# Kernel optimization log

Hardware: AMD Instinct MI355X
Metric: run time of the kernel (lower is better)

## Reference

```python
import jax, jax.numpy as jnp
import numpy as np

B, S, H, HD, DIM = 4, 4096, 32, 128, 4096
INTER = 11008
HC = 32          # heavy_channel_num
POS = 3000       # decode position
HEAVY = 256      # heavy_const (top-k keys kept)
BASE = 40000.0   # rope_base
EPS = 1e-5


def setup_inputs() -> dict:
    key = jax.random.key(0)
    ks = jax.random.split(key, 12)
    x = jax.random.normal(ks[0], (B, 1, DIM), jnp.float32)
    wqkv = jax.random.normal(ks[1], (3 * DIM, DIM), jnp.float32) * 0.02
    wo = jax.random.normal(ks[2], (DIM, DIM), jnp.float32) * 0.02
    w1 = jax.random.normal(ks[3], (INTER, DIM), jnp.float32) * 0.02
    w2 = jax.random.normal(ks[4], (DIM, INTER), jnp.float32) * 0.02
    w3 = jax.random.normal(ks[5], (INTER, DIM), jnp.float32) * 0.02
    attn_norm_w = jnp.ones((DIM,), jnp.float32)
    ffn_norm_w = jnp.ones((DIM,), jnp.float32)
    k_cache = jax.random.normal(ks[6], (B, S, H, HD), jnp.float32)
    v_cache = jax.random.normal(ks[7], (B, S, H, HD), jnp.float32)
    sorted_channel = jax.random.randint(ks[8], (H, HC), 0, HD).astype(jnp.int32)
    # k_label cache is consistent with k_cache gathered at the heavy channels
    k_label_cache = jnp.take_along_axis(k_cache, sorted_channel[None, None, :, :], axis=3)
    # rope freqs for the single decode position: [1, HD//2, 2] (cos, sin)
    inv = 1.0 / (BASE ** (np.arange(0, HD, 2, dtype=np.float32) / HD))
    ang = POS * inv
    freqs_cis = jnp.asarray(np.stack([np.cos(ang), np.sin(ang)], -1)[None], jnp.float32)
    # causal mask over cache positions (0 for valid, -1e9 beyond current pos)
    mask1 = jnp.where(jnp.arange(S) <= POS, 0.0, -1e9).astype(jnp.float32).reshape(1, 1, 1, S)
    return dict(x=x, wqkv=wqkv, wo=wo, w1=w1, w2=w2, w3=w3,
                attn_norm_w=attn_norm_w, ffn_norm_w=ffn_norm_w,
                k_cache=k_cache, v_cache=v_cache, k_label_cache=k_label_cache,
                freqs_cis=freqs_cis, mask1=mask1, sorted_channel=sorted_channel,
                input_pos=POS, heavy_const=HEAVY)


def rmsnorm(x, w):
    return x * jax.lax.rsqrt(jnp.mean(x * x, axis=-1, keepdims=True) + EPS) * w


def rope(x, fc):
    # x: [b, s, h, hd], fc: [s, hd//2, 2]
    xr = x.reshape(*x.shape[:-1], -1, 2)
    c = fc[None, :, None, :, 0]
    s = fc[None, :, None, :, 1]
    real = xr[..., 0] * c - xr[..., 1] * s
    imag = xr[..., 1] * c + xr[..., 0] * s
    return jnp.stack([real, imag], -1).reshape(x.shape)


def reference(x, wqkv, wo, w1, w2, w3, attn_norm_w, ffn_norm_w,
              k_cache, v_cache, k_label_cache, freqs_cis, mask1,
              sorted_channel, input_pos, heavy_const):
    xn = rmsnorm(x, attn_norm_w)
    qkv = xn @ wqkv.T                                   # [B,1,3*DIM]
    q, k, v = jnp.split(qkv, [DIM, 2 * DIM], axis=-1)
    q = rope(q.reshape(B, 1, H, HD), freqs_cis)
    k = rope(k.reshape(B, 1, H, HD), freqs_cis)
    v = v.reshape(B, 1, H, HD)
    # KVCache.update + k_label update
    k_cache = k_cache.at[:, input_pos].set(k[:, 0])
    v_cache = v_cache.at[:, input_pos].set(v[:, 0])
    k_lab = jnp.take_along_axis(k[:, 0], sorted_channel[None], axis=2)   # [B,H,HC]
    k_label_cache = k_label_cache.at[:, input_pos].set(k_lab)
    # heavy-channel label score + top-k key selection
    q_lab = jnp.take_along_axis(q[:, 0], sorted_channel[None], axis=2)   # [B,H,HC]
    label_scores = jnp.einsum('bhc,bshc->bhs', q_lab, k_label_cache) + mask1[0, 0]
    _, idx = jax.lax.top_k(label_scores, heavy_const)                    # [B,H,J]
    # fwd_sparse_no_mask: attention over only the selected keys
    kT = k_cache.transpose(0, 2, 1, 3)                                   # [B,H,S,HD]
    vT = v_cache.transpose(0, 2, 1, 3)
    k_sel = jnp.take_along_axis(kT, idx[..., None], axis=2)              # [B,H,J,HD]
    v_sel = jnp.take_along_axis(vT, idx[..., None], axis=2)
    att = jnp.einsum('bhd,bhjd->bhj', q[:, 0], k_sel) / np.float32(np.sqrt(HD))
    p = jax.nn.softmax(att.astype(jnp.float32), axis=-1).astype(q.dtype)
    o = jnp.einsum('bhj,bhjd->bhd', p, v_sel).reshape(B, 1, DIM)
    h = x + o @ wo.T
    hn = rmsnorm(h, ffn_norm_w)
    ffn = (jax.nn.silu(hn @ w1.T) * (hn @ w3.T)) @ w2.T
    return h + ffn
```

## Files before the change

### kernel.cpp

```cpp
#include <hip/hip_runtime.h>
#include <math.h>

#define NB 4
#define SEQ 4096
#define NH 32
#define HD 128
#define DIM 4096
#define INTER 11008
#define HC 32
#define HEAVY 256
#define EPS 1e-5f

typedef float f4 __attribute__((ext_vector_type(4)));

__device__ __forceinline__ float dotv(f4 a, f4 b) {
  f4 p = a * b;
  return p.x + p.y + p.z + p.w;
}
__device__ __forceinline__ f4 ld4(const float* p) { return *(const f4*)p; }
__device__ __forceinline__ f4 ldnt(const float* p) {
  return __builtin_nontemporal_load((const f4*)p);
}

__device__ __forceinline__ float wave_sum(float v) {
  #pragma unroll
  for (int off = 32; off; off >>= 1) v += __shfl_down(v, off, 64);
  return v;
}

template<int R>
__global__ __launch_bounds__(256) void qkv_norm_k(const float* __restrict__ w,
                                                  const float* __restrict__ x,
                                                  const float* __restrict__ nw,
                                                  float* __restrict__ out) {
  const int t = threadIdx.x;
  const int r0 = blockIdx.x * R;
  const int lane = t & 63, wi = t >> 6;
  __shared__ float redn[4][NB];
  __shared__ float red[4][R*NB];
  f4 xr[NB][4];
  #pragma unroll
  for (int b = 0; b < NB; ++b)
    #pragma unroll
    for (int j = 0; j < 4; ++j)
      xr[b][j] = ld4(x + b*DIM + (j*256 + t)*4);
  #pragma unroll
  for (int b = 0; b < NB; ++b) {
    float ss = 0.f;
    #pragma unroll
    for (int j = 0; j < 4; ++j) ss += dotv(xr[b][j], xr[b][j]);
    ss = wave_sum(ss);
    if (lane == 0) redn[wi][b] = ss;
  }
  #pragma unroll
  for (int j = 0; j < 4; ++j) {
    f4 aw = ld4(nw + (j*256 + t)*4);
    #pragma unroll
    for (int b = 0; b < NB; ++b) xr[b][j] *= aw;
  }
  float acc[R][NB];
  #pragma unroll
  for (int r = 0; r < R; ++r)
    #pragma unroll
    for (int b = 0; b < NB; ++b) acc[r][b] = 0.f;
  #pragma unroll
  for (int r = 0; r < R; ++r) {
    const float* wr = w + (size_t)(r0 + r) * DIM;
    #pragma unroll
    for (int j = 0; j < 4; ++j) {
      f4 wv = ld4(wr + (j*256 + t)*4);
      #pragma unroll
      for (int b = 0; b < NB; ++b) acc[r][b] += dotv(wv, xr[b][j]);
    }
  }
  #pragma unroll
  for (int r = 0; r < R; ++r)
    #pragma unroll
    for (int b = 0; b < NB; ++b) {
      float v = wave_sum(acc[r][b]);
      if (lane == 0) red[wi][r*NB + b] = v;
    }
  __syncthreads();
  if (t < R*NB) {
    int r = t >> 2, b = t & 3;
    float rs = rsqrtf((redn[0][b]+redn[1][b]+redn[2][b]+redn[3][b]) * (1.f/DIM) + EPS);
    float s = red[0][t] + red[1][t] + red[2][t] + red[3][t];
    out[(size_t)b*(3*DIM) + r0 + r] = rs * s;
  }
}

template<int R>
__global__ __launch_bounds__(256) void wo_k(const float* __restrict__ w,
                                            const float* __restrict__ x,
                                            const float* __restrict__ resid,
                                            float* __restrict__ out) {
  const int t = threadIdx.x;
  const int r0 = blockIdx.x * R;
  f4 xr[NB][4];
  #pragma unroll
  for (int b = 0; b < NB; ++b)
    #pragma unroll
    for (int j = 0; j < 4; ++j)
      xr[b][j] = ld4(x + b*DIM + (j*256 + t)*4);
  float acc[R][NB];
  #pragma unroll
  for (int r = 0; r < R; ++r)
    #pragma unroll
    for (int b = 0; b < NB; ++b) acc[r][b] = 0.f;
  #pragma unroll
  for (int r = 0; r < R; ++r) {
    const float* wr = w + (size_t)(r0 + r) * DIM;
    #pragma unroll
    for (int j = 0; j < 4; ++j) {
      f4 wv = ldnt(wr + (j*256 + t)*4);
      #pragma unroll
      for (int b = 0; b < NB; ++b) acc[r][b] += dotv(wv, xr[b][j]);
    }
  }
  __shared__ float red[4][R*NB];
  const int lane = t & 63, wi = t >> 6;
  #pragma unroll
  for (int r = 0; r < R; ++r)
    #pragma unroll
    for (int b = 0; b < NB; ++b) {
      float v = wave_sum(acc[r][b]);
      if (lane == 0) red[wi][r*NB + b] = v;
    }
  __syncthreads();
  if (t < R*NB) {
    int r = t >> 2, b = t & 3;
    float s = red[0][t] + red[1][t] + red[2][t] + red[3][t];
    out[(size_t)b*DIM + r0 + r] = resid[(size_t)b*DIM + r0 + r] + s;
  }
}

template<int R>
__global__ __launch_bounds__(256) void ffn13_norm_k(const float* __restrict__ w1,
                                                    const float* __restrict__ w3,
                                                    const float* __restrict__ h,
                                                    const float* __restrict__ nw,
                                                    float* __restrict__ g) {
  const int t = threadIdx.x;
  const int r0 = blockIdx.x * R;
  const int lane = t & 63, wi = t >> 6;
  __shared__ float redn[4][NB];
  __shared__ float red[4][2*R*NB];
  f4 xr[NB][4];
  #pragma unroll
  for (int b = 0; b < NB; ++b)
    #pragma unroll
    for (int j = 0; j < 4; ++j)
      xr[b][j] = ld4(h + b*DIM + (j*256 + t)*4);
  #pragma unroll
  for (int b = 0; b < NB; ++b) {
    float ss = 0.f;
    #pragma unroll
    for (int j = 0; j < 4; ++j) ss += dotv(xr[b][j], xr[b][j]);
    ss = wave_sum(ss);
    if (lane == 0) redn[wi][b] = ss;
  }
  #pragma unroll
  for (int j = 0; j < 4; ++j) {
    f4 aw = ld4(nw + (j*256 + t)*4);
    #pragma unroll
    for (int b = 0; b < NB; ++b) xr[b][j] *= aw;
  }
  float a1[R][NB], a3[R][NB];
  #pragma unroll
  for (int r = 0; r < R; ++r)
    #pragma unroll
    for (int b = 0; b < NB; ++b) { a1[r][b] = 0.f; a3[r][b] = 0.f; }
  #pragma unroll
  for (int r = 0; r < R; ++r) {
    const float* wr1 = w1 + (size_t)(r0 + r) * DIM;
    const float* wr3 = w3 + (size_t)(r0 + r) * DIM;
    #pragma unroll
    for (int j = 0; j < 4; ++j) {
      f4 v1 = ldnt(wr1 + (j*256 + t)*4);
      f4 v3 = ldnt(wr3 + (j*256 + t)*4);
      #pragma unroll
      for (int b = 0; b < NB; ++b) {
        a1[r][b] += dotv(v1, xr[b][j]);
        a3[r][b] += dotv(v3, xr[b][j]);
      }
    }
  }
  #pragma unroll
  for (int r = 0; r < R; ++r)
    #pragma unroll
    for (int b = 0; b < NB; ++b) {
      float v = wave_sum(a1[r][b]);
      if (lane == 0) red[wi][r*NB + b] = v;
      v = wave_sum(a3[r][b]);
      if (lane == 0) red[wi][R*NB + r*NB + b] = v;
    }
  __syncthreads();
  if (t < R*NB) {
    int r = t >> 2, b = t & 3;
    float rs = rsqrtf((redn[0][b]+redn[1][b]+redn[2][b]+redn[3][b]) * (1.f/DIM) + EPS);
    float d1 = rs * (red[0][t] + red[1][t] + red[2][t] + red[3][t]);
    int t3 = R*NB + t;
    float d3 = rs * (red[0][t3] + red[1][t3] + red[2][t3] + red[3][t3]);
    float s = d1 / (1.f + expf(-d1));
    g[(size_t)b*INTER + r0 + r] = s * d3;
  }
}

template<int R>
__global__ __launch_bounds__(256) void w2_k(const float* __restrict__ w2,
                                            const float* __restrict__ g,
                                            const float* __restrict__ h,
                                            float* __restrict__ out) {
  const int t = threadIdx.x;
  const int r0 = blockIdx.x * R;
  float acc[R][NB];
  #pragma unroll
  for (int r = 0; r < R; ++r)
    #pragma unroll
    for (int b = 0; b < NB; ++b) acc[r][b] = 0.f;
  #pragma unroll
  for (int i = 0; i < 11; ++i) {
    const int idx = t + i*256;
    if (idx < INTER/4) {
      f4 xv[NB];
      #pragma unroll
      for (int b = 0; b < NB; ++b) xv[b] = ld4(g + (size_t)b*INTER + idx*4);
      #pragma unroll
      for (int r = 0; r < R; ++r) {
        f4 wv = ldnt(w2 + (size_t)(r0 + r)*INTER + idx*4);
        #pragma unroll
        for (int b = 0; b < NB; ++b) acc[r][b] += dotv(wv, xv[b]);
      }
    }
  }
  __shared__ float red[4][R*NB];
  const int lane = t & 63, wi = t >> 6;
  #pragma unroll
  for (int r = 0; r < R; ++r)
    #pragma unroll
    for (int b = 0; b < NB; ++b) {
      float v = wave_sum(acc[r][b]);
      if (lane == 0) red[wi][r*NB + b] = v;
    }
  __syncthreads();
  if (t < R*NB) {
    int r = t >> 2, b = t & 3;
    float s = red[0][t] + red[1][t] + red[2][t] + red[3][t];
    out[(size_t)b*DIM + r0 + r] = h[(size_t)b*DIM + r0 + r] + s;
  }
}

__global__ __launch_bounds__(256) void scores_rope_k(const float* __restrict__ qkv,
                                                     const float* __restrict__ freqs,
                                                     const int* __restrict__ chan,
                                                     const float* __restrict__ klab_cache,
                                                     const int* __restrict__ pos_p,
                                                     uint32_t* __restrict__ su,
                                                     float* __restrict__ q_rot,
                                                     float* __restrict__ k_rot) {
  int bc = blockIdx.x; int c = bc & 3; int bh = bc >> 2;
  int b = bh >> 5, h = bh & 31;
  int pos = *pos_p; int n = pos + 1;
  int t = threadIdx.x;
  __shared__ float qs[HD], ks[HD], qv[HC], kls[HC];
  const float* qp = qkv + (size_t)b*3*DIM + h*HD;
  const float* kp = qp + DIM;
  if (t < 64) {
    float cc = freqs[2*t], sn = freqs[2*t+1];
    float q0 = qp[2*t], q1 = qp[2*t+1];
    float k0 = kp[2*t], k1 = kp[2*t+1];
    qs[2*t] = q0*cc - q1*sn; qs[2*t+1] = q1*cc + q0*sn;
    ks[2*t] = k0*cc - k1*sn; ks[2*t+1] = k1*cc + k0*sn;
  }
  __syncthreads();
  if (t < HC) { int ch = chan[h*HC + t]; qv[t] = qs[ch]; kls[t] = ks[ch]; }
  if (c == 0 && t < HD) {
    q_rot[(size_t)bh*HD + t] = qs[t];
    k_rot[(size_t)bh*HD + t] = ks[t];
  }
  __syncthreads();
  int chunk = (n + 3) >> 2;
  int s0 = c * chunk, s1 = min(n, s0 + chunk);
  for (int s = s0 + t; s < s1; s += 256) {
    float acc = 0.f;
    if (s == pos) {
      #pragma unroll
      for (int j = 0; j < HC; ++j) acc += qv[j] * kls[j];
    } else {
      const float* kl = klab_cache + (((size_t)b*SEQ + s)*NH + h)*HC;
      #pragma unroll
      for (int c4 = 0; c4 < HC/4; ++c4) {
        f4 kv = ld4(kl + c4*4);
        acc += qv[c4*4+0]*kv.x + qv[c4*4+1]*kv.y + qv[c4*4+2]*kv.z + qv[c4*4+3]*kv.w;
      }
    }
    uint32_t u = __float_as_uint(acc);
    u = (u & 0x80000000u) ? ~u : (u | 0x80000000u);
    su[(size_t)bh*SEQ + s] = u;
  }
}

__global__ __launch_bounds__(512) void selattn_k(const uint32_t* __restrict__ su_g,
                                                 const float* __restrict__ q_rot,
                                                 const float* __restrict__ k_rot,
                                                 const float* __restrict__ qkv,
                                                 const float* __restrict__ k_cache,
                                                 const float* __restrict__ v_cache,
                                                 const int* __restrict__ pos_p,
                                                 float* __restrict__ o) {
  const int bh = blockIdx.x, b = bh >> 5, h = bh & 31;
  const int pos = *pos_p, n = pos + 1;
  const int t = threadIdx.x;
  __shared__ uint32_t su[SEQ];
  __shared__ uint32_t hist[256], sfx[256];
  __shared__ uint32_t sh_prefix, sh_kremain, sh_cnt;
  __shared__ int lidx[HEAVY];
  __shared__ float sc[HEAVY], red8[8];
  __shared__ f4 qb4[HD/4], kb4[HD/4];
  __shared__ f4 ovv[16][32];
  __shared__ float s_m, s_sum;
  if (t == 0) { sh_prefix = 0; sh_kremain = HEAVY; sh_cnt = 0; }
  if (t < 32) { qb4[t] = ld4(q_rot + (size_t)bh*HD + t*4);
                kb4[t] = ld4(k_rot + (size_t)bh*HD + t*4); }
  for (int s = t; s < n; s += 512) su[s] = su_g[(size_t)bh*SEQ + s];
  __syncthreads();
  uint32_t prefix = 0;
  for (int pass = 0; pass < 4; ++pass) {
    int shift = 24 - 8*pass;
    if (t < 256) hist[t] = 0;
    __syncthreads();
    for (int s = t; s < n; s += 512) {
      uint32_t u = su[s];
      bool m = (pass == 0) || ((u >> (shift + 8)) == prefix);
      if (m) atomicAdd(&hist[(u >> shift) & 255u], 1u);
    }
    __syncthreads();
    uint32_t need = sh_kremain;
    if (t < 256) sfx[t] = hist[t];
    __syncthreads();
    #pragma unroll
    for (int off = 1; off < 256; off <<= 1) {
      uint32_t v = 0, a = 0;
      if (t < 256) { v = sfx[t]; a = (t + off < 256) ? sfx[t + off] : 0u; }
      __syncthreads();
      if (t < 256) sfx[t] = v + a;
      __syncthreads();
    }
    if (t < 256 && sfx[t] >= need && (t == 255 || sfx[t+1] < need)) {
      sh_prefix  = (prefix << 8) | (uint32_t)t;
      sh_kremain = need - ((t == 255) ? 0u : sfx[t+1]);
    }
    __syncthreads();
    prefix = sh_prefix;
  }
  const uint32_t T = prefix;
  for (int s = t; s < n; s += 512)
    if (su[s] > T) { uint32_t p = atomicAdd(&sh_cnt, 1u); lidx[p] = s; }
  __syncthreads();
  for (int s = t; s < n; s += 512)
    if (su[s] == T) {
      uint32_t p = atomicAdd(&sh_cnt, 1u);
      if (p < HEAVY) lidx[p] = s;
    }
  __syncthreads();
  {
    int j = t >> 1, half = t & 1;
    int s = lidx[j];
    float p;
    if (s == pos) {
      float a0 = 0.f;
      #pragma unroll
      for (int i = 0; i < 16; ++i)
        a0 += dotv(kb4[half*16 + i], qb4[half*16 + i]);
      p = a0;
    } else {
      const float* kk = k_cache + (((size_t)b*SEQ + s)*NH + h)*HD + half*64;
      float a0=0.f, a1=0.f, a2=0.f, a3=0.f;
      #pragma unroll
      for (int i = 0; i < 16; i += 4) {
        a0 += dotv(ldnt(kk + (i+0)*4), qb4[half*16 + i+0]);
        a1 += dotv(ldnt(kk + (i+1)*4), qb4[half*16 + i+1]);
        a2 += dotv(ldnt(kk + (i+2)*4), qb4[half*16 + i+2]);
        a3 += dotv(ldnt(kk + (i+3)*4), qb4[half*16 + i+3]);
      }
      p = (a0+a1)+(a2+a3);
    }
    p += __shfl_xor(p, 1, 64);
    if (half == 0) sc[j] = p * 0.088388347648318447f;
  }
  __syncthreads();
  float v = 0.f, p = 0.f, sum = 0.f;
  if (t < 256) {
    v = sc[t];
    float m = v;
    #pragma unroll
    for (int off = 32; off; off >>= 1) m = fmaxf(m, __shfl_xor(m, off, 64));
    if ((t & 63) == 0) red8[t >> 6] = m;
  }
  __syncthreads();
  if (t == 0) s_m = fmaxf(fmaxf(red8[0], red8[1]), fmaxf(red8[2], red8[3]));
  __syncthreads();
  if (t < 256) {
    p = expf(v - s_m);
    sum = p;
    #pragma unroll
    for (int off = 32; off; off >>= 1) sum += __shfl_xor(sum, off, 64);
    if ((t & 63) == 0) red8[4 + (t >> 6)] = sum;
  }
  __syncthreads();
  if (t == 0) s_sum = (red8[4] + red8[5]) + (red8[6] + red8[7]);
  __syncthreads();
  if (t < 256) sc[t] = p / s_sum;
  __syncthreads();
  {
    int d4 = t & 31, strm = t >> 5;
    const float* vnew = qkv + (size_t)b*3*DIM + 2*DIM + h*HD;
    f4 acc = {0.f, 0.f, 0.f, 0.f};
    for (int j = strm; j < HEAVY; j += 16) {
      int s = lidx[j];
      if (s == pos) acc += sc[j] * ld4(vnew + d4*4);
      else          acc += sc[j] * ldnt(v_cache + (((size_t)b*SEQ + s)*NH + h)*HD + d4*4);
    }
    ovv[strm][d4] = acc;
  }
  __syncthreads();
  if (t < 32) {
    f4 s = {0.f, 0.f, 0.f, 0.f};
    #pragma unroll
    for (int j = 0; j < 16; ++j) s += ovv[j][t];
    *(f4*)(o + (size_t)bh*HD + t*4) = s;
  }
}

extern "C" void kernel_launch(void* const* d_in, const int* in_sizes, int n_in,
                              void* d_out, int out_size, void* d_ws, size_t ws_size,
                              hipStream_t stream) {
  const float* x              = (const float*)d_in[0];
  const float* wqkv           = (const float*)d_in[1];
  const float* wo             = (const float*)d_in[2];
  const float* w1             = (const float*)d_in[3];
  const float* w2             = (const float*)d_in[4];
  const float* w3             = (const float*)d_in[5];
  const float* attn_norm_w    = (const float*)d_in[6];
  const float* ffn_norm_w     = (const float*)d_in[7];
  const float* k_cache        = (const float*)d_in[8];
  const float* v_cache        = (const float*)d_in[9];
  const float* k_label_cache  = (const float*)d_in[10];
  const float* freqs          = (const float*)d_in[11];
  const int*   sorted_channel = (const int*)d_in[13];
  const int*   pos_p          = (const int*)d_in[14];

  float* ws    = (float*)d_ws;
  float* qkv   = ws;
  float* q_rot = qkv + NB*3*DIM;
  float* k_rot = q_rot + NB*NH*HD;
  float* o     = k_rot + NB*NH*HD;
  float* h     = o + NB*DIM;
  float* g     = h + NB*DIM;
  uint32_t* su = (uint32_t*)(g + NB*INTER);

  qkv_norm_k<2>  <<<3*DIM/2, 256, 0, stream>>>(wqkv, x, attn_norm_w, qkv);
  scores_rope_k  <<<NB*NH*4, 256, 0, stream>>>(qkv, freqs, sorted_channel,
                                               k_label_cache, pos_p, su, q_rot, k_rot);
  selattn_k      <<<NB*NH,   512, 0, stream>>>(su, q_rot, k_rot, qkv,
                                               k_cache, v_cache, pos_p, o);
  wo_k<2>        <<<DIM/2,   256, 0, stream>>>(wo, o, x, h);
  ffn13_norm_k<2><<<INTER/2, 256, 0, stream>>>(w1, w3, h, ffn_norm_w, g);
  w2_k<2>        <<<DIM/2,   256, 0, stream>>>(w2, g, h, (float*)d_out);
}
```

Baseline: 239.4 us.

## Use grid-stride persistent loops in GEMV kernels and drop nontemporal KV loads

The QKV, WO and FFN13 GEMV kernels now run a grid-stride loop over row chunks with fewer blocks. Each block loads and normalizes the activation vector once and reuses it across several chunks, which amortizes that per-block setup. The shared reduction buffers are double-buffered by parity so consecutive iterations avoid an extra barrier. Separately, the sparse-attention gathers of K and V switch from nontemporal loads to ordinary cached loads, and the V load is merged into one pointer-select path.

```diff
diff --git a/kernel.cpp b/kernel.cpp
--- a/kernel.cpp
+++ b/kernel.cpp
@@ -32,12 +32,12 @@
 __global__ __launch_bounds__(256) void qkv_norm_k(const float* __restrict__ w,
                                                   const float* __restrict__ x,
                                                   const float* __restrict__ nw,
-                                                  float* __restrict__ out) {
+                                                  float* __restrict__ out,
+                                                  int nch) {
   const int t = threadIdx.x;
-  const int r0 = blockIdx.x * R;
   const int lane = t & 63, wi = t >> 6;
   __shared__ float redn[4][NB];
-  __shared__ float red[4][R*NB];
+  __shared__ float red[2][4][R*NB];
   f4 xr[NB][4];
   #pragma unroll
   for (int b = 0; b < NB; ++b)
@@ -58,34 +58,38 @@
     #pragma unroll
     for (int b = 0; b < NB; ++b) xr[b][j] *= aw;
   }
-  float acc[R][NB];
-  #pragma unroll
-  for (int r = 0; r < R; ++r)
-    #pragma unroll
-    for (int b = 0; b < NB; ++b) acc[r][b] = 0.f;
-  #pragma unroll
-  for (int r = 0; r < R; ++r) {
-    const float* wr = w + (size_t)(r0 + r) * DIM;
-    #pragma unroll
-    for (int j = 0; j < 4; ++j) {
-      f4 wv = ld4(wr + (j*256 + t)*4);
-      #pragma unroll
-      for (int b = 0; b < NB; ++b) acc[r][b] += dotv(wv, xr[b][j]);
-    }
-  }
-  #pragma unroll
-  for (int r = 0; r < R; ++r)
-    #pragma unroll
-    for (int b = 0; b < NB; ++b) {
-      float v = wave_sum(acc[r][b]);
-      if (lane == 0) red[wi][r*NB + b] = v;
-    }
-  __syncthreads();
-  if (t < R*NB) {
-    int r = t >> 2, b = t & 3;
-    float rs = rsqrtf((redn[0][b]+redn[1][b]+redn[2][b]+redn[3][b]) * (1.f/DIM) + EPS);
-    float s = red[0][t] + red[1][t] + red[2][t] + red[3][t];
-    out[(size_t)b*(3*DIM) + r0 + r] = rs * s;
+  int parity = 0;
+  for (int ch = blockIdx.x; ch < nch; ch += gridDim.x, parity ^= 1) {
+    const int r0 = ch * R;
+    float acc[R][NB];
+    #pragma unroll
+    for (int r = 0; r < R; ++r)
+      #pragma unroll
+      for (int b = 0; b < NB; ++b) acc[r][b] = 0.f;
+    #pragma unroll
+    for (int r = 0; r < R; ++r) {
+      const float* wr = w + (size_t)(r0 + r) * DIM;
+      #pragma unroll
+      for (int j = 0; j < 4; ++j) {
+        f4 wv = ld4(wr + (j*256 + t)*4);
+        #pragma unroll
+        for (int b = 0; b < NB; ++b) acc[r][b] += dotv(wv, xr[b][j]);
+      }
+    }
+    #pragma unroll
+    for (int r = 0; r < R; ++r)
+      #pragma unroll
+      for (int b = 0; b < NB; ++b) {
+        float v = wave_sum(acc[r][b]);
+        if (lane == 0) red[parity][wi][r*NB + b] = v;
+      }
+    __syncthreads();
+    if (t < R*NB) {
+      int r = t >> 2, b = t & 3;
+      float rs = rsqrtf((redn[0][b]+redn[1][b]+redn[2][b]+redn[3][b]) * (1.f/DIM) + EPS);
+      float s = red[parity][0][t] + red[parity][1][t] + red[parity][2][t] + red[parity][3][t];
+      out[(size_t)b*(3*DIM) + r0 + r] = rs * s;
+    }
   }
 }
 
@@ -93,44 +97,48 @@
 __global__ __launch_bounds__(256) void wo_k(const float* __restrict__ w,
                                             const float* __restrict__ x,
                                             const float* __restrict__ resid,
-                                            float* __restrict__ out) {
+                                            float* __restrict__ out,
+                                            int nch) {
   const int t = threadIdx.x;
-  const int r0 = blockIdx.x * R;
+  const int lane = t & 63, wi = t >> 6;
+  __shared__ float red[2][4][R*NB];
   f4 xr[NB][4];
   #pragma unroll
   for (int b = 0; b < NB; ++b)
     #pragma unroll
     for (int j = 0; j < 4; ++j)
       xr[b][j] = ld4(x + b*DIM + (j*256 + t)*4);
-  float acc[R][NB];
-  #pragma unroll
-  for (int r = 0; r < R; ++r)
-    #pragma unroll
-    for (int b = 0; b < NB; ++b) acc[r][b] = 0.f;
-  #pragma unroll
-  for (int r = 0; r < R; ++r) {
-    const float* wr = w + (size_t)(r0 + r) * DIM;
-    #pragma unroll
-    for (int j = 0; j < 4; ++j) {
-      f4 wv = ldnt(wr + (j*256 + t)*4);
-      #pragma unroll
-      for (int b = 0; b < NB; ++b) acc[r][b] += dotv(wv, xr[b][j]);
-    }
-  }
-  __shared__ float red[4][R*NB];
-  const int lane = t & 63, wi = t >> 6;
-  #pragma unroll
-  for (int r = 0; r < R; ++r)
-    #pragma unroll
-    for (int b = 0; b < NB; ++b) {
-      float v = wave_sum(acc[r][b]);
-      if (lane == 0) red[wi][r*NB + b] = v;
-    }
-  __syncthreads();
-  if (t < R*NB) {
-    int r = t >> 2, b = t & 3;
-    float s = red[0][t] + red[1][t] + red[2][t] + red[3][t];
-    out[(size_t)b*DIM + r0 + r] = resid[(size_t)b*DIM + r0 + r] + s;
+  int parity = 0;
+  for (int ch = blockIdx.x; ch < nch; ch += gridDim.x, parity ^= 1) {
+    const int r0 = ch * R;
+    float acc[R][NB];
+    #pragma unroll
+    for (int r = 0; r < R; ++r)
+      #pragma unroll
+      for (int b = 0; b < NB; ++b) acc[r][b] = 0.f;
+    #pragma unroll
+    for (int r = 0; r < R; ++r) {
+      const float* wr = w + (size_t)(r0 + r) * DIM;
+      #pragma unroll
+      for (int j = 0; j < 4; ++j) {
+        f4 wv = ldnt(wr + (j*256 + t)*4);
+        #pragma unroll
+        for (int b = 0; b < NB; ++b) acc[r][b] += dotv(wv, xr[b][j]);
+      }
+    }
+    #pragma unroll
+    for (int r = 0; r < R; ++r)
+      #pragma unroll
+      for (int b = 0; b < NB; ++b) {
+        float v = wave_sum(acc[r][b]);
+        if (lane == 0) red[parity][wi][r*NB + b] = v;
+      }
+    __syncthreads();
+    if (t < R*NB) {
+      int r = t >> 2, b = t & 3;
+      float s = red[parity][0][t] + red[parity][1][t] + red[parity][2][t] + red[parity][3][t];
+      out[(size_t)b*DIM + r0 + r] = resid[(size_t)b*DIM + r0 + r] + s;
+    }
   }
 }
 
@@ -139,12 +147,12 @@
                                                     const float* __restrict__ w3,
                                                     const float* __restrict__ h,
                                                     const float* __restrict__ nw,
-                                                    float* __restrict__ g) {
+                                                    float* __restrict__ g,
+                                                    int nch) {
   const int t = threadIdx.x;
-  const int r0 = blockIdx.x * R;
   const int lane = t & 63, wi = t >> 6;
   __shared__ float redn[4][NB];
-  __shared__ float red[4][2*R*NB];
+  __shared__ float red[2][4][2*R*NB];
   f4 xr[NB][4];
   #pragma unroll
   for (int b = 0; b < NB; ++b)
@@ -165,44 +173,48 @@
     #pragma unroll
     for (int b = 0; b < NB; ++b) xr[b][j] *= aw;
   }
-  float a1[R][NB], a3[R][NB];
-  #pragma unroll
-  for (int r = 0; r < R; ++r)
-    #pragma unroll
-    for (int b = 0; b < NB; ++b) { a1[r][b] = 0.f; a3[r][b] = 0.f; }
-  #pragma unroll
-  for (int r = 0; r < R; ++r) {
-    const float* wr1 = w1 + (size_t)(r0 + r) * DIM;
-    const float* wr3 = w3 + (size_t)(r0 + r) * DIM;
-    #pragma unroll
-    for (int j = 0; j < 4; ++j) {
-      f4 v1 = ldnt(wr1 + (j*256 + t)*4);
-      f4 v3 = ldnt(wr3 + (j*256 + t)*4);
+  int parity = 0;
+  for (int ch = blockIdx.x; ch < nch; ch += gridDim.x, parity ^= 1) {
+    const int r0 = ch * R;
+    float a1[R][NB], a3[R][NB];
+    #pragma unroll
+    for (int r = 0; r < R; ++r)
+      #pragma unroll
+      for (int b = 0; b < NB; ++b) { a1[r][b] = 0.f; a3[r][b] = 0.f; }
+    #pragma unroll
+    for (int r = 0; r < R; ++r) {
+      const float* wr1 = w1 + (size_t)(r0 + r) * DIM;
+      const float* wr3 = w3 + (size_t)(r0 + r) * DIM;
+      #pragma unroll
+      for (int j = 0; j < 4; ++j) {
+        f4 v1 = ldnt(wr1 + (j*256 + t)*4);
+        f4 v3 = ldnt(wr3 + (j*256 + t)*4);
+        #pragma unroll
+        for (int b = 0; b < NB; ++b) {
+          a1[r][b] += dotv(v1, xr[b][j]);
+          a3[r][b] += dotv(v3, xr[b][j]);
+        }
+      }
+    }
+    #pragma unroll
+    for (int r = 0; r < R; ++r)
       #pragma unroll
       for (int b = 0; b < NB; ++b) {
-        a1[r][b] += dotv(v1, xr[b][j]);
-        a3[r][b] += dotv(v3, xr[b][j]);
-      }
-    }
-  }
-  #pragma unroll
-  for (int r = 0; r < R; ++r)
-    #pragma unroll
-    for (int b = 0; b < NB; ++b) {
-      float v = wave_sum(a1[r][b]);
-      if (lane == 0) red[wi][r*NB + b] = v;
-      v = wave_sum(a3[r][b]);
-      if (lane == 0) red[wi][R*NB + r*NB + b] = v;
-    }
-  __syncthreads();
-  if (t < R*NB) {
-    int r = t >> 2, b = t & 3;
-    float rs = rsqrtf((redn[0][b]+redn[1][b]+redn[2][b]+redn[3][b]) * (1.f/DIM) + EPS);
-    float d1 = rs * (red[0][t] + red[1][t] + red[2][t] + red[3][t]);
-    int t3 = R*NB + t;
-    float d3 = rs * (red[0][t3] + red[1][t3] + red[2][t3] + red[3][t3]);
-    float s = d1 / (1.f + expf(-d1));
-    g[(size_t)b*INTER + r0 + r] = s * d3;
+        float v = wave_sum(a1[r][b]);
+        if (lane == 0) red[parity][wi][r*NB + b] = v;
+        v = wave_sum(a3[r][b]);
+        if (lane == 0) red[parity][wi][R*NB + r*NB + b] = v;
+      }
+    __syncthreads();
+    if (t < R*NB) {
+      int r = t >> 2, b = t & 3;
+      float rs = rsqrtf((redn[0][b]+redn[1][b]+redn[2][b]+redn[3][b]) * (1.f/DIM) + EPS);
+      float d1 = rs * (red[parity][0][t] + red[parity][1][t] + red[parity][2][t] + red[parity][3][t]);
+      int t3 = R*NB + t;
+      float d3 = rs * (red[parity][0][t3] + red[parity][1][t3] + red[parity][2][t3] + red[parity][3][t3]);
+      float s = d1 / (1.f + expf(-d1));
+      g[(size_t)b*INTER + r0 + r] = s * d3;
+    }
   }
 }
 
@@ -378,10 +390,10 @@
       float a0=0.f, a1=0.f, a2=0.f, a3=0.f;
       #pragma unroll
       for (int i = 0; i < 16; i += 4) {
-        a0 += dotv(ldnt(kk + (i+0)*4), qb4[half*16 + i+0]);
-        a1 += dotv(ldnt(kk + (i+1)*4), qb4[half*16 + i+1]);
-        a2 += dotv(ldnt(kk + (i+2)*4), qb4[half*16 + i+2]);
-        a3 += dotv(ldnt(kk + (i+3)*4), qb4[half*16 + i+3]);
+        a0 += dotv(ld4(kk + (i+0)*4), qb4[half*16 + i+0]);
+        a1 += dotv(ld4(kk + (i+1)*4), qb4[half*16 + i+1]);
+        a2 += dotv(ld4(kk + (i+2)*4), qb4[half*16 + i+2]);
+        a3 += dotv(ld4(kk + (i+3)*4), qb4[half*16 + i+3]);
       }
       p = (a0+a1)+(a2+a3);
     }
@@ -418,8 +430,9 @@
     f4 acc = {0.f, 0.f, 0.f, 0.f};
     for (int j = strm; j < HEAVY; j += 16) {
       int s = lidx[j];
-      if (s == pos) acc += sc[j] * ld4(vnew + d4*4);
-      else          acc += sc[j] * ldnt(v_cache + (((size_t)b*SEQ + s)*NH + h)*HD + d4*4);
+      const float* vp = (s == pos) ? vnew
+                                   : (v_cache + (((size_t)b*SEQ + s)*NH + h)*HD);
+      acc += sc[j] * ld4(vp + d4*4);
     }
     ovv[strm][d4] = acc;
   }
@@ -459,12 +472,12 @@
   float* g     = h + NB*DIM;
   uint32_t* su = (uint32_t*)(g + NB*INTER);
 
-  qkv_norm_k<2>  <<<3*DIM/2, 256, 0, stream>>>(wqkv, x, attn_norm_w, qkv);
+  qkv_norm_k<2>  <<<2048,    256, 0, stream>>>(wqkv, x, attn_norm_w, qkv, 3*DIM/2);
   scores_rope_k  <<<NB*NH*4, 256, 0, stream>>>(qkv, freqs, sorted_channel,
                                                k_label_cache, pos_p, su, q_rot, k_rot);
   selattn_k      <<<NB*NH,   512, 0, stream>>>(su, q_rot, k_rot, qkv,
                                                k_cache, v_cache, pos_p, o);
-  wo_k<2>        <<<DIM/2,   256, 0, stream>>>(wo, o, x, h);
-  ffn13_norm_k<2><<<INTER/2, 256, 0, stream>>>(w1, w3, h, ffn_norm_w, g);
+  wo_k<2>        <<<1024,    256, 0, stream>>>(wo, o, x, h, DIM/2);
+  ffn13_norm_k<2><<<2048,    256, 0, stream>>>(w1, w3, h, ffn_norm_w, g, INTER/2);
   w2_k<2>        <<<DIM/2,   256, 0, stream>>>(w2, g, h, (float*)d_out);
 }
```

New measurement: 212.3 us. -11.3%, faster.
